# Performance work log

Hardware: AMD Instinct MI355X
Metric: run time of the kernel (lower is better)

## Reference

```python
import jax, jax.numpy as jnp
import numpy as np

DT = 1.0 / 60.0  # physics timestep
NUM_BODY = 20

# ---- quaternion helpers (xyzw convention, matching the repo) ----

def quat_from_rotvec(rv):
    # rv: [..., 3] axis-angle -> quaternion [..., 4] (x,y,z,w)
    angle = jnp.linalg.norm(rv, axis=-1, keepdims=True)
    half = 0.5 * angle
    safe = jnp.where(angle < 1e-8, 1.0, angle)
    s = jnp.where(angle < 1e-8, 0.5 - angle * angle / 48.0, jnp.sin(half) / safe)
    return jnp.concatenate([rv * s, jnp.cos(half)], axis=-1)


def flip_quat_by_w(q):
    return jnp.where(q[..., 3:4] < 0, -q, q)


def quat_to_vec6d(q):
    # first two columns of the rotation matrix, row-major flattened -> [..., 6]
    x, y, z, w = q[..., 0], q[..., 1], q[..., 2], q[..., 3]
    r00 = 1 - 2 * (y * y + z * z)
    r10 = 2 * (x * y + z * w)
    r20 = 2 * (x * z - y * w)
    r01 = 2 * (x * y - z * w)
    r11 = 1 - 2 * (x * x + z * z)
    r21 = 2 * (y * z + x * w)
    return jnp.stack([r00, r01, r10, r11, r20, r21], axis=-1)


def quat_apply(q, v):
    # rotate v [..., 3] by quaternion q [..., 4]; broadcasts over leading dims
    xyz, w = q[..., :3], q[..., 3:4]
    t = 2.0 * jnp.cross(xyz, v)
    return v + w * t + jnp.cross(xyz, t)


def quat_multiply(p, q):
    pv, pw = p[..., :3], p[..., 3:4]
    qv, qw = q[..., :3], q[..., 3:4]
    v = pw * qv + qw * pv + jnp.cross(pv, qv)
    w = pw * qw - jnp.sum(pv * qv, axis=-1, keepdims=True)
    return jnp.concatenate([v, w], axis=-1)


def quat_integrate(q, omega, dt):
    # q_{t+1} = normalize(q + 0.5*dt * (omega_quat * q))
    omega_q = jnp.concatenate([omega, jnp.zeros_like(omega[..., :1])], axis=-1)
    dq = quat_multiply(omega_q, q)
    r = q + 0.5 * dt * dq
    return r / jnp.linalg.norm(r, axis=-1, keepdims=True)


def integrate_state(state, delta, dt):
    # state: [B, NB, 13] = pos(3) | rot quat(4) | vel(3) | avel(3)
    B, NB, _ = state.shape
    pos, rot = state[..., 0:3], state[..., 3:7]
    vel, avel = state[..., 7:10], state[..., 10:13]
    root_rot = state[:, 0:1, 3:7]                       # [B, 1, 4]
    d3 = delta.reshape(B, -1, 3)                        # [B, 2*NB, 3]
    true_d = quat_apply(root_rot, d3).reshape(B, NB, 6)
    lin, ang = true_d[..., :3], true_d[..., 3:]
    next_vel = vel + lin
    next_avel = avel + ang
    next_pos = pos + next_vel * dt
    next_rot = quat_integrate(rot, next_avel, dt)
    return jnp.concatenate([next_pos, next_rot, next_vel, next_avel], axis=-1)


def setup_inputs() -> dict:
    key = jax.random.key(0)
    ks = jax.random.split(key, 12)
    B = 32768
    inp = {
        "state": jax.random.normal(ks[0], (B, NUM_BODY, 13), jnp.float32),
        "action": jax.random.normal(ks[1], (B, 57), jnp.float32),
        "n_observation": jax.random.normal(ks[2], (B, 300), jnp.float32),
        "W1": jax.random.normal(ks[3], (414, 512), jnp.float32) * 0.05,
        "b1": jax.random.normal(ks[4], (512,), jnp.float32) * 0.05,
        "W2": jax.random.normal(ks[5], (512, 512), jnp.float32) * 0.05,
        "b2": jax.random.normal(ks[6], (512,), jnp.float32) * 0.05,
        "W3": jax.random.normal(ks[7], (512, 120), jnp.float32) * 0.05,
        "b3": jax.random.normal(ks[8], (120,), jnp.float32) * 0.05,
        "delta_mean": jax.random.normal(ks[9], (120,), jnp.float32) * 0.01,
        "delta_std": jax.random.uniform(ks[10], (120,), jnp.float32) + 0.5,
    }
    return inp


def reference(state, action, n_observation, W1, b1, W2, b2, W3, b3, delta_mean, delta_std):
    B = action.shape[0]
    # action rotvecs -> quats -> 6d representation
    aq = flip_quat_by_w(quat_from_rotvec(action.reshape(-1, 3)))
    a6 = quat_to_vec6d(aq).reshape(B, -1)               # [B, 114]
    x = jnp.concatenate([n_observation, a6], axis=-1)   # [B, 414]
    h = jax.nn.relu(x @ W1 + b1)
    h = jax.nn.relu(h @ W2 + b2)
    n_delta = h @ W3 + b3                                # [B, 120]
    delta = n_delta * delta_std + delta_mean             # unnormalize
    return integrate_state(state, delta, DT)
```

## Files before the change

### kernel.cpp

```cpp
#include <hip/hip_runtime.h>
#include <hip/hip_bf16.h>
#include <math.h>

#define DT (1.0f / 60.0f)

typedef __bf16 bf16x8 __attribute__((ext_vector_type(8)));
typedef float f32x4 __attribute__((ext_vector_type(4)));

#define XSTRIDE 848
#define HSTRIDE 1040

struct __attribute__((packed)) f4u {
    float x, y, z, w;
};

__global__ __launch_bounds__(256) void prep_weights(
    const float* __restrict__ W1, const float* __restrict__ W2,
    const float* __restrict__ W3, __hip_bfloat16* __restrict__ W1p,
    __hip_bfloat16* __restrict__ W2p, __hip_bfloat16* __restrict__ W3p) {
    int idx = blockIdx.x * 256 + threadIdx.x;
    if (idx < 212992) {
        int d = idx;
        int e = d & 7, l = (d >> 3) & 63, t = d >> 9;
        int nt = t & 31, ks = t >> 5;
        int n = nt * 16 + (l & 15);
        int k = ks * 32 + (l >> 4) * 8 + e;
        W1p[d] = __float2bfloat16(k < 414 ? W1[k * 512 + n] : 0.0f);
        return;
    }
    idx -= 212992;
    if (idx < 262144) {
        int d = idx;
        int e = d & 7, l = (d >> 3) & 63, t = d >> 9;
        int nt = t & 31, ks = t >> 5;
        int n = nt * 16 + (l & 15);
        int k = ks * 32 + (l >> 4) * 8 + e;
        W2p[d] = __float2bfloat16(W2[k * 512 + n]);
        return;
    }
    idx -= 262144;
    if (idx < 65536) {
        int d = idx;
        int e = d & 7, l = (d >> 3) & 63, t = d >> 9;
        int nt = t & 7, ks = t >> 3;
        int n = nt * 16 + (l & 15);
        int k = ks * 32 + (l >> 4) * 8 + e;
        W3p[d] = __float2bfloat16(n < 120 ? W3[k * 120 + n] : 0.0f);
    }
}

template <int KSTEPS, int NT, int JF, int ASTRIDE>
__device__ __forceinline__ void mlp_layer(const char* Abase, const char* Bbase,
                                          int laneOff, f32x4 (&acc)[4][JF]) {
    bf16x8 w0[JF], w1[JF];
#pragma unroll
    for (int j = 0; j < JF; j++)
        w0[j] = *(const bf16x8*)(Bbase + (j << 10) + laneOff);
#pragma unroll 2
    for (int ks = 0; ks < KSTEPS; ks++) {
        if (ks + 1 < KSTEPS) {
            if ((ks & 1) == 0) {
#pragma unroll
                for (int j = 0; j < JF; j++)
                    w1[j] = *(const bf16x8*)(Bbase + (((ks + 1) * NT + j) << 10) + laneOff);
            } else {
#pragma unroll
                for (int j = 0; j < JF; j++)
                    w0[j] = *(const bf16x8*)(Bbase + (((ks + 1) * NT + j) << 10) + laneOff);
            }
        }
        bf16x8 ax[4];
#pragma unroll
        for (int i = 0; i < 4; i++)
            ax[i] = *(const bf16x8*)(Abase + ks * 64 + i * 16 * ASTRIDE);
#pragma unroll
        for (int i = 0; i < 4; i++)
#pragma unroll
            for (int j = 0; j < JF; j++)
                acc[i][j] = __builtin_amdgcn_mfma_f32_16x16x32_bf16(
                    (ks & 1) ? w1[j] : w0[j], ax[i], acc[i][j], 0, 0, 0);
    }
}

__device__ __forceinline__ void store_h_relu_t(const f32x4 (&acc)[4][4],
                                               char* smem, const float* bias,
                                               int wn, int lrow, int kgrp) {
#pragma unroll
    for (int j = 0; j < 4; j++) {
        int f = wn * 64 + j * 16 + kgrp * 4;
        float4 bb = *(const float4*)(bias + f);
#pragma unroll
        for (int i = 0; i < 4; i++) {
            float v0 = acc[i][j][0] + bb.x;
            float v1 = acc[i][j][1] + bb.y;
            float v2 = acc[i][j][2] + bb.z;
            float v3 = acc[i][j][3] + bb.w;
            v0 = v0 > 0.0f ? v0 : 0.0f;
            v1 = v1 > 0.0f ? v1 : 0.0f;
            v2 = v2 > 0.0f ? v2 : 0.0f;
            v3 = v3 > 0.0f ? v3 : 0.0f;
            union { __hip_bfloat162 h2[2]; uint2 u; } pk;
            pk.h2[0] = __float22bfloat162_rn(make_float2(v0, v1));
            pk.h2[1] = __float22bfloat162_rn(make_float2(v2, v3));
            *(uint2*)(smem + (i * 16 + lrow) * HSTRIDE + f * 2) = pk.u;
        }
    }
}

__device__ __forceinline__ void quat_apply3(float qx, float qy, float qz,
                                            float qw, float vx, float vy,
                                            float vz, float& ox, float& oy,
                                            float& oz) {
    float tx = 2.0f * (qy * vz - qz * vy);
    float ty = 2.0f * (qz * vx - qx * vz);
    float tz = 2.0f * (qx * vy - qy * vx);
    ox = vx + qw * tx + (qy * tz - qz * ty);
    oy = vy + qw * ty + (qz * tx - qx * tz);
    oz = vz + qw * tz + (qx * ty - qy * tx);
}

__global__ __launch_bounds__(512, 4) void fused_mlp(
    const float* __restrict__ obs, const float* __restrict__ action,
    const __hip_bfloat16* __restrict__ W1p, const float* __restrict__ b1,
    const __hip_bfloat16* __restrict__ W2p, const float* __restrict__ b2,
    const __hip_bfloat16* __restrict__ W3p, const float* __restrict__ b3,
    const float* __restrict__ dstd, const float* __restrict__ dmean,
    const float* __restrict__ state, float* __restrict__ out) {
    alignas(16) __shared__ char smem[64 * HSTRIDE];
    const int tid = threadIdx.x;
    const int blk = blockIdx.x;
    const int lane = tid & 63, wn = tid >> 6;
    const int lrow = lane & 15, kgrp = lane >> 4;
    const int laneOff = lane * 16;

    {
        const float4* og = (const float4*)obs + (size_t)blk * 64 * 75;
#pragma unroll
        for (int i = 0; i < 10; i++) {
            int f = tid + i * 512;
            if (f < 4800) {
                int row = f / 75;
                int c4 = f - row * 75;
                float4 v = og[f];
                union { __hip_bfloat162 h2[2]; uint2 u; } pk;
                pk.h2[0] = __float22bfloat162_rn(make_float2(v.x, v.y));
                pk.h2[1] = __float22bfloat162_rn(make_float2(v.z, v.w));
                *(uint2*)(smem + row * XSTRIDE + c4 * 8) = pk.u;
            }
        }
#pragma unroll
        for (int i = 0; i < 3; i++) {
            int q = tid + i * 512;
            if (q < 1216) {
                int row = q / 19;
                int j = q - row * 19;
                const float* a = action + ((size_t)(blk * 64 + row)) * 57 + j * 3;
                float rx = a[0], ry = a[1], rz = a[2];
                float ang = sqrtf(rx * rx + ry * ry + rz * rz);
                float half = 0.5f * ang;
                float s;
                if (ang < 1e-8f)
                    s = 0.5f - ang * ang * (1.0f / 48.0f);
                else
                    s = sinf(half) / ang;
                float qx = rx * s, qy = ry * s, qz = rz * s, qw = cosf(half);
                union { __hip_bfloat16 h[6]; uint u[3]; } pq;
                pq.h[0] = __float2bfloat16(1.0f - 2.0f * (qy * qy + qz * qz));
                pq.h[1] = __float2bfloat16(2.0f * (qx * qy - qz * qw));
                pq.h[2] = __float2bfloat16(2.0f * (qx * qy + qz * qw));
                pq.h[3] = __float2bfloat16(1.0f - 2.0f * (qx * qx + qz * qz));
                pq.h[4] = __float2bfloat16(2.0f * (qx * qz - qy * qw));
                pq.h[5] = __float2bfloat16(2.0f * (qy * qz + qx * qw));
                char* p = smem + row * XSTRIDE + 600 + j * 12;
                *(uint*)p = pq.u[0];
                *(uint*)(p + 4) = pq.u[1];
                *(uint*)(p + 8) = pq.u[2];
            }
        }
        if (tid < 320) {
            int row = tid / 5;
            int p = tid - row * 5;
            *(uint*)(smem + row * XSTRIDE + 828 + p * 4) = 0u;
        }
    }
    __syncthreads();

    f32x4 acc[4][4];
    f32x4 zero4 = {0.0f, 0.0f, 0.0f, 0.0f};
#pragma unroll
    for (int i = 0; i < 4; i++)
#pragma unroll
        for (int j = 0; j < 4; j++) acc[i][j] = zero4;

    mlp_layer<13, 32, 4, XSTRIDE>(smem + lrow * XSTRIDE + kgrp * 16,
                                  (const char*)W1p + (wn << 12), laneOff, acc);
    __syncthreads();
    store_h_relu_t(acc, smem, b1, wn, lrow, kgrp);
    __syncthreads();

#pragma unroll
    for (int i = 0; i < 4; i++)
#pragma unroll
        for (int j = 0; j < 4; j++) acc[i][j] = zero4;
    mlp_layer<16, 32, 4, HSTRIDE>(smem + lrow * HSTRIDE + kgrp * 16,
                                  (const char*)W2p + (wn << 12), laneOff, acc);
    __syncthreads();
    store_h_relu_t(acc, smem, b2, wn, lrow, kgrp);
    __syncthreads();

    f4u ps0[3], ps1[3], ps2[3], prq[3];
    float ps12[3];
#pragma unroll
    for (int it = 0; it < 3; it++) {
        int idx = tid + it * 512;
        if (idx < 1280) {
            int lr = idx / 20;
            int body = idx - lr * 20;
            const float* sb = state + ((size_t)(blk * 64 + lr)) * 260 + body * 13;
            const float* rq = state + ((size_t)(blk * 64 + lr)) * 260 + 3;
            ps0[it] = *(const f4u*)sb;
            ps1[it] = *(const f4u*)(sb + 4);
            ps2[it] = *(const f4u*)(sb + 8);
            ps12[it] = sb[12];
            prq[it] = *(const f4u*)rq;
        }
    }

    f32x4 a3[4];
#pragma unroll
    for (int i = 0; i < 4; i++) a3[i] = zero4;
    {
        const char* Ab = smem + lrow * HSTRIDE + kgrp * 16;
        const char* Bb = (const char*)W3p + (wn << 10);
        bf16x8 c0 = *(const bf16x8*)(Bb + laneOff);
        bf16x8 c1;
#pragma unroll 2
        for (int ks = 0; ks < 16; ks++) {
            if (ks + 1 < 16) {
                if ((ks & 1) == 0)
                    c1 = *(const bf16x8*)(Bb + ((ks + 1) << 13) + laneOff);
                else
                    c0 = *(const bf16x8*)(Bb + ((ks + 1) << 13) + laneOff);
            }
            bf16x8 ax[4];
#pragma unroll
            for (int i = 0; i < 4; i++)
                ax[i] = *(const bf16x8*)(Ab + ks * 64 + i * 16 * HSTRIDE);
#pragma unroll
            for (int i = 0; i < 4; i++)
                a3[i] = __builtin_amdgcn_mfma_f32_16x16x32_bf16(
                    (ks & 1) ? c1 : c0, ax[i], a3[i], 0, 0, 0);
        }
    }
    __syncthreads();

    float* dl = (float*)smem;
    {
        int f = wn * 16 + kgrp * 4;
        if (f < 120) {
            float4 bb = *(const float4*)(b3 + f);
            float4 sc = *(const float4*)(dstd + f);
            float4 mn = *(const float4*)(dmean + f);
#pragma unroll
            for (int i = 0; i < 4; i++) {
                int row = i * 16 + lrow;
                float4 dv;
                dv.x = (a3[i][0] + bb.x) * sc.x + mn.x;
                dv.y = (a3[i][1] + bb.y) * sc.y + mn.y;
                dv.z = (a3[i][2] + bb.z) * sc.z + mn.z;
                dv.w = (a3[i][3] + bb.w) * sc.w + mn.w;
                *(float4*)(dl + row * 120 + f) = dv;
            }
        }
    }
    __syncthreads();

#pragma unroll
    for (int it = 0; it < 3; it++) {
        int idx = tid + it * 512;
        if (idx < 1280) {
            int lr = idx / 20;
            int body = idx - lr * 20;
            int rowg = blk * 64 + lr;
            float qx = prq[it].x, qy = prq[it].y, qz = prq[it].z, qw = prq[it].w;
            const float* d = dl + lr * 120 + body * 6;

            float lx, ly, lz, ax, ay, az;
            quat_apply3(qx, qy, qz, qw, d[0], d[1], d[2], lx, ly, lz);
            quat_apply3(qx, qy, qz, qw, d[3], d[4], d[5], ax, ay, az);

            float vx = ps1[it].w + lx, vy = ps2[it].x + ly, vz = ps2[it].y + lz;
            float wx = ps2[it].z + ax, wy = ps2[it].w + ay, wz = ps12[it] + az;
            float px = ps0[it].x + vx * DT, py = ps0[it].y + vy * DT,
                  pz = ps0[it].z + vz * DT;

            float rx = ps0[it].w, ry = ps1[it].x, rz = ps1[it].y, rw = ps1[it].z;
            float dqx = rw * wx + (wy * rz - wz * ry);
            float dqy = rw * wy + (wz * rx - wx * rz);
            float dqz = rw * wz + (wx * ry - wy * rx);
            float dqw = -(wx * rx + wy * ry + wz * rz);
            float h = 0.5f * DT;
            float nx = rx + h * dqx, ny = ry + h * dqy, nz = rz + h * dqz,
                  nw = rw + h * dqw;
            float inv = 1.0f / sqrtf(nx * nx + ny * ny + nz * nz + nw * nw);

            float* o = out + (size_t)rowg * 260 + body * 13;
            o[0] = px;
            o[1] = py;
            o[2] = pz;
            o[3] = nx * inv;
            o[4] = ny * inv;
            o[5] = nz * inv;
            o[6] = nw * inv;
            o[7] = vx;
            o[8] = vy;
            o[9] = vz;
            o[10] = wx;
            o[11] = wy;
            o[12] = wz;
        }
    }
}

extern "C" void kernel_launch(void* const* d_in, const int* in_sizes, int n_in,
                              void* d_out, int out_size, void* d_ws,
                              size_t ws_size, hipStream_t stream) {
    const float* state = (const float*)d_in[0];
    const float* action = (const float*)d_in[1];
    const float* obs = (const float*)d_in[2];
    const float* W1 = (const float*)d_in[3];
    const float* b1 = (const float*)d_in[4];
    const float* W2 = (const float*)d_in[5];
    const float* b2 = (const float*)d_in[6];
    const float* W3 = (const float*)d_in[7];
    const float* b3 = (const float*)d_in[8];
    const float* dmean = (const float*)d_in[9];
    const float* dstd = (const float*)d_in[10];
    float* out = (float*)d_out;
    char* ws = (char*)d_ws;

    const int B = in_sizes[1] / 57;

    __hip_bfloat16* W1p = (__hip_bfloat16*)(ws);
    __hip_bfloat16* W2p = (__hip_bfloat16*)(ws + 425984);
    __hip_bfloat16* W3p = (__hip_bfloat16*)(ws + 950272);

    prep_weights<<<2112, 256, 0, stream>>>(W1, W2, W3, W1p, W2p, W3p);
    fused_mlp<<<B / 64, 512, 0, stream>>>(obs, action, W1p, b1, W2p, b2, W3p,
                                          b3, dstd, dmean, state, out);
}
```

Before: 166.9 us.

## Process 128 rows per block with 1024 threads to share weight loads

Each block now handles 128 batch rows with 16 waves arranged as 2 row groups by 8 feature groups, instead of 64 rows with 8 waves. Waves in different row groups load the same weight fragments, so weight traffic per row through the cache is halved. The action sin/cos also switch to fast intrinsics. The cost is a larger LDS footprint (about 133KB per block), fewer blocks per CU, and half as many blocks overall, which may hurt occupancy and load balance; the kernel also assumes B is divisible by 128.

```diff
diff --git a/kernel.cpp b/kernel.cpp
--- a/kernel.cpp
+++ b/kernel.cpp
@@ -9,6 +9,7 @@
 
 #define XSTRIDE 848
 #define HSTRIDE 1040
+#define ROWS 128
 
 struct __attribute__((packed)) f4u {
     float x, y, z, w;
@@ -84,10 +85,11 @@
 
 __device__ __forceinline__ void store_h_relu_t(const f32x4 (&acc)[4][4],
                                                char* smem, const float* bias,
-                                               int wn, int lrow, int kgrp) {
+                                               int rg, int fg, int lrow,
+                                               int kgrp) {
 #pragma unroll
     for (int j = 0; j < 4; j++) {
-        int f = wn * 64 + j * 16 + kgrp * 4;
+        int f = fg * 64 + j * 16 + kgrp * 4;
         float4 bb = *(const float4*)(bias + f);
 #pragma unroll
         for (int i = 0; i < 4; i++) {
@@ -102,7 +104,7 @@
             union { __hip_bfloat162 h2[2]; uint2 u; } pk;
             pk.h2[0] = __float22bfloat162_rn(make_float2(v0, v1));
             pk.h2[1] = __float22bfloat162_rn(make_float2(v2, v3));
-            *(uint2*)(smem + (i * 16 + lrow) * HSTRIDE + f * 2) = pk.u;
+            *(uint2*)(smem + (rg * 64 + i * 16 + lrow) * HSTRIDE + f * 2) = pk.u;
         }
     }
 }
@@ -119,26 +121,27 @@
     oz = vz + qw * tz + (qx * ty - qy * tx);
 }
 
-__global__ __launch_bounds__(512, 4) void fused_mlp(
+__global__ __launch_bounds__(1024, 4) void fused_mlp(
     const float* __restrict__ obs, const float* __restrict__ action,
     const __hip_bfloat16* __restrict__ W1p, const float* __restrict__ b1,
     const __hip_bfloat16* __restrict__ W2p, const float* __restrict__ b2,
     const __hip_bfloat16* __restrict__ W3p, const float* __restrict__ b3,
     const float* __restrict__ dstd, const float* __restrict__ dmean,
     const float* __restrict__ state, float* __restrict__ out) {
-    alignas(16) __shared__ char smem[64 * HSTRIDE];
+    alignas(16) __shared__ char smem[ROWS * HSTRIDE];
     const int tid = threadIdx.x;
     const int blk = blockIdx.x;
     const int lane = tid & 63, wn = tid >> 6;
+    const int rg = wn >> 3, fg = wn & 7;
     const int lrow = lane & 15, kgrp = lane >> 4;
     const int laneOff = lane * 16;
 
     {
-        const float4* og = (const float4*)obs + (size_t)blk * 64 * 75;
+        const float4* og = (const float4*)obs + (size_t)blk * ROWS * 75;
 #pragma unroll
         for (int i = 0; i < 10; i++) {
-            int f = tid + i * 512;
-            if (f < 4800) {
+            int f = tid + i * 1024;
+            if (f < ROWS * 75) {
                 int row = f / 75;
                 int c4 = f - row * 75;
                 float4 v = og[f];
@@ -150,11 +153,11 @@
         }
 #pragma unroll
         for (int i = 0; i < 3; i++) {
-            int q = tid + i * 512;
-            if (q < 1216) {
+            int q = tid + i * 1024;
+            if (q < ROWS * 19) {
                 int row = q / 19;
                 int j = q - row * 19;
-                const float* a = action + ((size_t)(blk * 64 + row)) * 57 + j * 3;
+                const float* a = action + ((size_t)(blk * ROWS + row)) * 57 + j * 3;
                 float rx = a[0], ry = a[1], rz = a[2];
                 float ang = sqrtf(rx * rx + ry * ry + rz * rz);
                 float half = 0.5f * ang;
@@ -162,8 +165,8 @@
                 if (ang < 1e-8f)
                     s = 0.5f - ang * ang * (1.0f / 48.0f);
                 else
-                    s = sinf(half) / ang;
-                float qx = rx * s, qy = ry * s, qz = rz * s, qw = cosf(half);
+                    s = __sinf(half) / ang;
+                float qx = rx * s, qy = ry * s, qz = rz * s, qw = __cosf(half);
                 union { __hip_bfloat16 h[6]; uint u[3]; } pq;
                 pq.h[0] = __float2bfloat16(1.0f - 2.0f * (qy * qy + qz * qz));
                 pq.h[1] = __float2bfloat16(2.0f * (qx * qy - qz * qw));
@@ -177,7 +180,7 @@
                 *(uint*)(p + 8) = pq.u[2];
             }
         }
-        if (tid < 320) {
+        if (tid < ROWS * 5) {
             int row = tid / 5;
             int p = tid - row * 5;
             *(uint*)(smem + row * XSTRIDE + 828 + p * 4) = 0u;
@@ -192,32 +195,34 @@
 #pragma unroll
         for (int j = 0; j < 4; j++) acc[i][j] = zero4;
 
-    mlp_layer<13, 32, 4, XSTRIDE>(smem + lrow * XSTRIDE + kgrp * 16,
-                                  (const char*)W1p + (wn << 12), laneOff, acc);
-    __syncthreads();
-    store_h_relu_t(acc, smem, b1, wn, lrow, kgrp);
+    mlp_layer<13, 32, 4, XSTRIDE>(
+        smem + (rg * 64 + lrow) * XSTRIDE + kgrp * 16,
+        (const char*)W1p + (fg << 12), laneOff, acc);
+    __syncthreads();
+    store_h_relu_t(acc, smem, b1, rg, fg, lrow, kgrp);
     __syncthreads();
 
 #pragma unroll
     for (int i = 0; i < 4; i++)
 #pragma unroll
         for (int j = 0; j < 4; j++) acc[i][j] = zero4;
-    mlp_layer<16, 32, 4, HSTRIDE>(smem + lrow * HSTRIDE + kgrp * 16,
-                                  (const char*)W2p + (wn << 12), laneOff, acc);
-    __syncthreads();
-    store_h_relu_t(acc, smem, b2, wn, lrow, kgrp);
+    mlp_layer<16, 32, 4, HSTRIDE>(
+        smem + (rg * 64 + lrow) * HSTRIDE + kgrp * 16,
+        (const char*)W2p + (fg << 12), laneOff, acc);
+    __syncthreads();
+    store_h_relu_t(acc, smem, b2, rg, fg, lrow, kgrp);
     __syncthreads();
 
     f4u ps0[3], ps1[3], ps2[3], prq[3];
     float ps12[3];
 #pragma unroll
     for (int it = 0; it < 3; it++) {
-        int idx = tid + it * 512;
-        if (idx < 1280) {
+        int idx = tid + it * 1024;
+        if (idx < ROWS * 20) {
             int lr = idx / 20;
             int body = idx - lr * 20;
-            const float* sb = state + ((size_t)(blk * 64 + lr)) * 260 + body * 13;
-            const float* rq = state + ((size_t)(blk * 64 + lr)) * 260 + 3;
+            const float* sb = state + ((size_t)(blk * ROWS + lr)) * 260 + body * 13;
+            const float* rq = state + ((size_t)(blk * ROWS + lr)) * 260 + 3;
             ps0[it] = *(const f4u*)sb;
             ps1[it] = *(const f4u*)(sb + 4);
             ps2[it] = *(const f4u*)(sb + 8);
@@ -230,8 +235,8 @@
 #pragma unroll
     for (int i = 0; i < 4; i++) a3[i] = zero4;
     {
-        const char* Ab = smem + lrow * HSTRIDE + kgrp * 16;
-        const char* Bb = (const char*)W3p + (wn << 10);
+        const char* Ab = smem + (rg * 64 + lrow) * HSTRIDE + kgrp * 16;
+        const char* Bb = (const char*)W3p + (fg << 10);
         bf16x8 c0 = *(const bf16x8*)(Bb + laneOff);
         bf16x8 c1;
 #pragma unroll 2
@@ -256,14 +261,14 @@
 
     float* dl = (float*)smem;
     {
-        int f = wn * 16 + kgrp * 4;
+        int f = fg * 16 + kgrp * 4;
         if (f < 120) {
             float4 bb = *(const float4*)(b3 + f);
             float4 sc = *(const float4*)(dstd + f);
             float4 mn = *(const float4*)(dmean + f);
 #pragma unroll
             for (int i = 0; i < 4; i++) {
-                int row = i * 16 + lrow;
+                int row = rg * 64 + i * 16 + lrow;
                 float4 dv;
                 dv.x = (a3[i][0] + bb.x) * sc.x + mn.x;
                 dv.y = (a3[i][1] + bb.y) * sc.y + mn.y;
@@ -277,11 +282,11 @@
 
 #pragma unroll
     for (int it = 0; it < 3; it++) {
-        int idx = tid + it * 512;
-        if (idx < 1280) {
+        int idx = tid + it * 1024;
+        if (idx < ROWS * 20) {
             int lr = idx / 20;
             int body = idx - lr * 20;
-            int rowg = blk * 64 + lr;
+            int rowg = blk * ROWS + lr;
             float qx = prq[it].x, qy = prq[it].y, qz = prq[it].z, qw = prq[it].w;
             const float* d = dl + lr * 120 + body * 6;
 
@@ -346,6 +351,6 @@
     __hip_bfloat16* W3p = (__hip_bfloat16*)(ws + 950272);
 
     prep_weights<<<2112, 256, 0, stream>>>(W1, W2, W3, W1p, W2p, W3p);
-    fused_mlp<<<B / 64, 512, 0, stream>>>(obs, action, W1p, b1, W2p, b2, W3p,
-                                          b3, dstd, dmean, state, out);
-}
+    fused_mlp<<<B / ROWS, 1024, 0, stream>>>(obs, action, W1p, b1, W2p, b2,
+                                             W3p, b3, dstd, dmean, state, out);
+}
```

Result: slower. 171.4 us (+2.7%).

## Prefetch next-layer weights early, stage output through LDS for coalesced stores

Applied to the files above, without the earlier changes.

Issues the first weight-fragment loads for W1, W2 and W3 ahead of the preceding barriers and epilogues so their global latency overlaps other work. Output rows are written to shared memory and then stored as contiguous float4 writes instead of scattered per-thread 13-float stores. The delta buffer gets a padded stride to reduce LDS bank conflicts, and sin/cos switch to fast intrinsics. It adds register pressure from the prefetched fragments and the 39-float output staging array, plus extra barriers.

```diff
diff --git a/kernel.cpp b/kernel.cpp
--- a/kernel.cpp
+++ b/kernel.cpp
@@ -9,6 +9,7 @@
 
 #define XSTRIDE 848
 #define HSTRIDE 1040
+#define DLSTRIDE 124
 
 struct __attribute__((packed)) f4u {
     float x, y, z, w;
@@ -51,11 +52,11 @@
 
 template <int KSTEPS, int NT, int JF, int ASTRIDE>
 __device__ __forceinline__ void mlp_layer(const char* Abase, const char* Bbase,
-                                          int laneOff, f32x4 (&acc)[4][JF]) {
+                                          int laneOff, f32x4 (&acc)[4][JF],
+                                          bf16x8 (&wpre)[JF]) {
     bf16x8 w0[JF], w1[JF];
 #pragma unroll
-    for (int j = 0; j < JF; j++)
-        w0[j] = *(const bf16x8*)(Bbase + (j << 10) + laneOff);
+    for (int j = 0; j < JF; j++) w0[j] = wpre[j];
 #pragma unroll 2
     for (int ks = 0; ks < KSTEPS; ks++) {
         if (ks + 1 < KSTEPS) {
@@ -133,6 +134,11 @@
     const int lrow = lane & 15, kgrp = lane >> 4;
     const int laneOff = lane * 16;
 
+    bf16x8 wpre[4];
+#pragma unroll
+    for (int j = 0; j < 4; j++)
+        wpre[j] = *(const bf16x8*)((const char*)W1p + (wn << 12) + (j << 10) + laneOff);
+
     {
         const float4* og = (const float4*)obs + (size_t)blk * 64 * 75;
 #pragma unroll
@@ -162,8 +168,8 @@
                 if (ang < 1e-8f)
                     s = 0.5f - ang * ang * (1.0f / 48.0f);
                 else
-                    s = sinf(half) / ang;
-                float qx = rx * s, qy = ry * s, qz = rz * s, qw = cosf(half);
+                    s = __sinf(half) / ang;
+                float qx = rx * s, qy = ry * s, qz = rz * s, qw = __cosf(half);
                 union { __hip_bfloat16 h[6]; uint u[3]; } pq;
                 pq.h[0] = __float2bfloat16(1.0f - 2.0f * (qy * qy + qz * qz));
                 pq.h[1] = __float2bfloat16(2.0f * (qx * qy - qz * qw));
@@ -193,7 +199,11 @@
         for (int j = 0; j < 4; j++) acc[i][j] = zero4;
 
     mlp_layer<13, 32, 4, XSTRIDE>(smem + lrow * XSTRIDE + kgrp * 16,
-                                  (const char*)W1p + (wn << 12), laneOff, acc);
+                                  (const char*)W1p + (wn << 12), laneOff, acc,
+                                  wpre);
+#pragma unroll
+    for (int j = 0; j < 4; j++)
+        wpre[j] = *(const bf16x8*)((const char*)W2p + (wn << 12) + (j << 10) + laneOff);
     __syncthreads();
     store_h_relu_t(acc, smem, b1, wn, lrow, kgrp);
     __syncthreads();
@@ -203,7 +213,10 @@
 #pragma unroll
         for (int j = 0; j < 4; j++) acc[i][j] = zero4;
     mlp_layer<16, 32, 4, HSTRIDE>(smem + lrow * HSTRIDE + kgrp * 16,
-                                  (const char*)W2p + (wn << 12), laneOff, acc);
+                                  (const char*)W2p + (wn << 12), laneOff, acc,
+                                  wpre);
+    const char* Bb3 = (const char*)W3p + (wn << 10);
+    bf16x8 c0 = *(const bf16x8*)(Bb3 + laneOff);
     __syncthreads();
     store_h_relu_t(acc, smem, b2, wn, lrow, kgrp);
     __syncthreads();
@@ -231,16 +244,14 @@
     for (int i = 0; i < 4; i++) a3[i] = zero4;
     {
         const char* Ab = smem + lrow * HSTRIDE + kgrp * 16;
-        const char* Bb = (const char*)W3p + (wn << 10);
-        bf16x8 c0 = *(const bf16x8*)(Bb + laneOff);
         bf16x8 c1;
 #pragma unroll 2
         for (int ks = 0; ks < 16; ks++) {
             if (ks + 1 < 16) {
                 if ((ks & 1) == 0)
-                    c1 = *(const bf16x8*)(Bb + ((ks + 1) << 13) + laneOff);
+                    c1 = *(const bf16x8*)(Bb3 + ((ks + 1) << 13) + laneOff);
                 else
-                    c0 = *(const bf16x8*)(Bb + ((ks + 1) << 13) + laneOff);
+                    c0 = *(const bf16x8*)(Bb3 + ((ks + 1) << 13) + laneOff);
             }
             bf16x8 ax[4];
 #pragma unroll
@@ -269,21 +280,21 @@
                 dv.y = (a3[i][1] + bb.y) * sc.y + mn.y;
                 dv.z = (a3[i][2] + bb.z) * sc.z + mn.z;
                 dv.w = (a3[i][3] + bb.w) * sc.w + mn.w;
-                *(float4*)(dl + row * 120 + f) = dv;
-            }
-        }
-    }
-    __syncthreads();
-
+                *(float4*)(dl + row * DLSTRIDE + f) = dv;
+            }
+        }
+    }
+    __syncthreads();
+
+    float ov[3][13];
 #pragma unroll
     for (int it = 0; it < 3; it++) {
         int idx = tid + it * 512;
         if (idx < 1280) {
             int lr = idx / 20;
             int body = idx - lr * 20;
-            int rowg = blk * 64 + lr;
             float qx = prq[it].x, qy = prq[it].y, qz = prq[it].z, qw = prq[it].w;
-            const float* d = dl + lr * 120 + body * 6;
+            const float* d = dl + lr * DLSTRIDE + body * 6;
 
             float lx, ly, lz, ax, ay, az;
             quat_apply3(qx, qy, qz, qw, d[0], d[1], d[2], lx, ly, lz);
@@ -304,20 +315,44 @@
                   nw = rw + h * dqw;
             float inv = 1.0f / sqrtf(nx * nx + ny * ny + nz * nz + nw * nw);
 
-            float* o = out + (size_t)rowg * 260 + body * 13;
-            o[0] = px;
-            o[1] = py;
-            o[2] = pz;
-            o[3] = nx * inv;
-            o[4] = ny * inv;
-            o[5] = nz * inv;
-            o[6] = nw * inv;
-            o[7] = vx;
-            o[8] = vy;
-            o[9] = vz;
-            o[10] = wx;
-            o[11] = wy;
-            o[12] = wz;
+            ov[it][0] = px;
+            ov[it][1] = py;
+            ov[it][2] = pz;
+            ov[it][3] = nx * inv;
+            ov[it][4] = ny * inv;
+            ov[it][5] = nz * inv;
+            ov[it][6] = nw * inv;
+            ov[it][7] = vx;
+            ov[it][8] = vy;
+            ov[it][9] = vz;
+            ov[it][10] = wx;
+            ov[it][11] = wy;
+            ov[it][12] = wz;
+        }
+    }
+    __syncthreads();
+
+#pragma unroll
+    for (int it = 0; it < 3; it++) {
+        int idx = tid + it * 512;
+        if (idx < 1280) {
+            int lr = idx / 20;
+            int body = idx - lr * 20;
+            float* dst = (float*)(smem + lr * 1040 + body * 52);
+#pragma unroll
+            for (int k = 0; k < 13; k++) dst[k] = ov[it][k];
+        }
+    }
+    __syncthreads();
+
+    {
+        float4* og = (float4*)(out + (size_t)blk * 64 * 260);
+#pragma unroll
+        for (int i = 0; i < 9; i++) {
+            int f = tid + i * 512;
+            if (f < 4160) {
+                og[f] = *(const float4*)(smem + f * 16);
+            }
         }
     }
 }
```

After: 162.9 us. 1.02x faster.
